# Kernel optimization log

Measured on AMD Instinct MI355X. Metric: run time of the kernel, lower is better.

Reference implementation:

```python
import jax, jax.numpy as jnp
import numpy as np

MARGIN = 0.2  # args.margin
N, D, NUM_CLASSES = 512, 256, 32


def setup_inputs() -> dict:
    key = jax.random.key(0)
    k1, k2 = jax.random.split(key)
    embeddings = jax.random.normal(k1, (N, D), dtype=jnp.float32)
    labels = jax.random.randint(k2, (N,), 0, NUM_CLASSES, dtype=jnp.int64)
    return {"embeddings": embeddings, "labels": labels}


def reference(embeddings, labels):
    """TripletMarginMiner forward (type_of_triplets='all', euclidean, no l2 norm).

    torch version returns variable-length (anchor, pos, neg) index vectors;
    for jit-compatibility we return the equivalent fixed-shape [N,N,N] boolean
    mask M where M[a,p,n]=True iff (a,p,n) is a mined triplet. The torch output
    is exactly jnp.where(M).
    """
    emb = jax.lax.stop_gradient(embeddings)  # embeddings.detach()

    # pairwise squared-euclidean distance matrix [N, N]
    sq = jnp.sum(emb * emb, axis=1)
    mat = jnp.maximum(sq[:, None] + sq[None, :] - 2.0 * (emb @ emb.T), 0.0)

    # label structure
    sames = labels[:, None] == labels[None, :]          # [N, N]
    diffs = ~sames
    sames = sames & ~jnp.eye(labels.shape[0], dtype=bool)  # fill_diagonal_(0)
    valid = sames[:, :, None] & diffs[:, None, :]        # [a, p, n]

    # triplet_margin[a,p,n] = an_dist - ap_dist = mat[a,n] - mat[a,p]
    triplet_margin = mat[:, None, :] - mat[:, :, None]   # [a, p, n]

    # type_of_triplets == 'all': margin violators
    mask = valid & (triplet_margin <= MARGIN)
    return mask
```

## Files before the change

### kernel.cpp

```cpp
#include <hip/hip_runtime.h>

#pragma clang fp contract(off)

#define NN 512
#define DD 256

typedef int int4v __attribute__((ext_vector_type(4)));

__device__ __forceinline__ float np_leaf128_avx512(const float* __restrict__ x)
{
    float p[16];
    #pragma unroll
    for (int i = 0; i < 16; ++i) {
        const float q0 = x[i]       * x[i];
        const float q1 = x[i + 16]  * x[i + 16];
        const float q2 = x[i + 32]  * x[i + 32];
        const float q3 = x[i + 48]  * x[i + 48];
        const float q4 = x[i + 64]  * x[i + 64];
        const float q5 = x[i + 80]  * x[i + 80];
        const float q6 = x[i + 96]  * x[i + 96];
        const float q7 = x[i + 112] * x[i + 112];
        p[i] = ((q0 + q1) + (q2 + q3)) + ((q4 + q5) + (q6 + q7));
    }
    float q[8];
    #pragma unroll
    for (int i = 0; i < 8; ++i) q[i] = p[i] + p[i + 8];
    const float s0 = q[0] + q[4];
    const float s1 = q[1] + q[5];
    const float s2 = q[2] + q[6];
    const float s3 = q[3] + q[7];
    const float u0 = s0 + s2;
    const float u1 = s1 + s3;
    return u0 + u1;
}

__global__ __launch_bounds__(512)
void triplet_kernel(const float* __restrict__ emb,
                    const int* __restrict__ lab,
                    int* __restrict__ out)
{
    __shared__ int   canon[NN];
    __shared__ float arow[DD];
    __shared__ float dn[NN];
    __shared__ float mp[NN];
    __shared__ float sq_a_sh;
    __shared__ int   det_lab64;

    const int a = blockIdx.x;
    const int t = threadIdx.x;

    if (t == 0) det_lab64 = 0;
    __syncthreads();
    if (t < 256 && lab[2 * t + 1] == 0) atomicAdd(&det_lab64, 1);
    __syncthreads();
    canon[t] = (det_lab64 == 256) ? lab[2 * t] : lab[t];

    if (t < DD) arow[t] = emb[(size_t)a * DD + t];
    __syncthreads();

    const float* __restrict__ xr = emb + (size_t)t * DD;
    const float sqj = np_leaf128_avx512(xr) + np_leaf128_avx512(xr + 128);
    if (t == a) sq_a_sh = sqj;

    float dot = 0.0f;
    for (int k = 0; k < DD; ++k)
        dot = __builtin_fmaf(arow[k], xr[k], dot);
    __syncthreads();

    const float t1 = sq_a_sh + sqj;
    const float t2 = 2.0f * dot;
    float m = t1 - t2;
    m = m > 0.0f ? m : 0.0f;

    const int la = canon[a];
    dn[t] = (canon[t] != la) ? m : __builtin_inff();
    mp[t] = (canon[t] == la && t != a) ? m : __builtin_nanf("");
    __syncthreads();

    const int tx = t & 127;
    const int ty = t >> 7;
    const float d0 = dn[4 * tx + 0];
    const float d1 = dn[4 * tx + 1];
    const float d2 = dn[4 * tx + 2];
    const float d3 = dn[4 * tx + 3];

    int4v* base = (int4v*)out + (size_t)a * NN * (NN / 4) + tx;
    for (int p = ty; p < NN; p += 4) {
        const float mpp = mp[p];
        int4v r;
        r.x = ((d0 - mpp) <= 0.2f) ? 1 : 0;
        r.y = ((d1 - mpp) <= 0.2f) ? 1 : 0;
        r.z = ((d2 - mpp) <= 0.2f) ? 1 : 0;
        r.w = ((d3 - mpp) <= 0.2f) ? 1 : 0;
        base[(size_t)p * (NN / 4)] = r;
    }
}

extern "C" void kernel_launch(void* const* d_in, const int* in_sizes, int n_in,
                              void* d_out, int out_size, void* d_ws, size_t ws_size,
                              hipStream_t stream)
{
    const float* emb    = (const float*)d_in[0];
    const int*   labels = (const int*)d_in[1];
    int*         out    = (int*)d_out;
    (void)d_ws; (void)ws_size;

    triplet_kernel<<<NN, 512, 0, stream>>>(emb, labels, out);
}
```

Before: 569.7 us.

## Split triplet mask into distance-table kernel and widely parallel mask-writing kernel

Splits the fused kernel in two. The first kernel computes per-anchor negative and positive distance tables into workspace. The second launches 4096 blocks of 256 threads, each writing a 64-row chunk of the 512MB output mask. This spreads the dominant output write over many more blocks than the original 512, aiming to raise memory-level parallelism. In exchange it adds a second launch and a round trip of the tables through workspace, and it falls back to the fused kernel when the workspace is too small.

```diff
diff --git a/kernel.cpp b/kernel.cpp
--- a/kernel.cpp
+++ b/kernel.cpp
@@ -4,10 +4,11 @@
 
 #define NN 512
 #define DD 256
+#define PCH 64
 
 typedef int int4v __attribute__((ext_vector_type(4)));
 
-__device__ __forceinline__ float np_leaf128_avx512(const float* __restrict__ x)
+__device__ __forceinline__ float np_leaf128(const float* __restrict__ x)
 {
     float p[16];
     #pragma unroll
@@ -29,15 +30,94 @@
     const float s1 = q[1] + q[5];
     const float s2 = q[2] + q[6];
     const float s3 = q[3] + q[7];
-    const float u0 = s0 + s2;
-    const float u1 = s1 + s3;
-    return u0 + u1;
+    return (s0 + s2) + (s1 + s3);
 }
 
 __global__ __launch_bounds__(512)
-void triplet_kernel(const float* __restrict__ emb,
-                    const int* __restrict__ lab,
-                    int* __restrict__ out)
+void tables_kernel(const float* __restrict__ emb,
+                   const int* __restrict__ lab,
+                   float* __restrict__ dn_ws,
+                   float* __restrict__ mp_ws)
+{
+    __shared__ int   canon[NN];
+    __shared__ float arow[DD];
+    __shared__ float sq_a_sh;
+    __shared__ int   det_lab64;
+
+    const int a = blockIdx.x;
+    const int t = threadIdx.x;
+
+    if (t == 0) det_lab64 = 0;
+    __syncthreads();
+    if (t < 256 && lab[2 * t + 1] == 0) atomicAdd(&det_lab64, 1);
+    __syncthreads();
+    canon[t] = (det_lab64 == 256) ? lab[2 * t] : lab[t];
+
+    if (t < DD) arow[t] = emb[(size_t)a * DD + t];
+    __syncthreads();
+
+    const float* __restrict__ xr = emb + (size_t)t * DD;
+    const float sqj = np_leaf128(xr) + np_leaf128(xr + 128);
+    if (t == a) sq_a_sh = sqj;
+
+    float dot = 0.0f;
+    for (int k = 0; k < DD; ++k)
+        dot = __builtin_fmaf(arow[k], xr[k], dot);
+    __syncthreads();
+
+    const float t1 = sq_a_sh + sqj;
+    const float t2 = 2.0f * dot;
+    float m = t1 - t2;
+    m = m > 0.0f ? m : 0.0f;
+
+    const int la = canon[a];
+    dn_ws[(size_t)a * NN + t] = (canon[t] != la) ? m : __builtin_inff();
+    mp_ws[(size_t)a * NN + t] = (canon[t] == la && t != a) ? m
+                                                           : __builtin_nanf("");
+}
+
+__global__ __launch_bounds__(256)
+void mask_kernel(const float* __restrict__ dn_ws,
+                 const float* __restrict__ mp_ws,
+                 int* __restrict__ out)
+{
+    __shared__ float dn_sh[NN];
+    __shared__ float mp_sh[PCH];
+
+    const int bid = blockIdx.x;
+    const int a   = bid >> 3;
+    const int pc  = bid & 7;
+    const int t   = threadIdx.x;
+
+    dn_sh[t]       = dn_ws[(size_t)a * NN + t];
+    dn_sh[t + 256] = dn_ws[(size_t)a * NN + t + 256];
+    if (t < PCH) mp_sh[t] = mp_ws[(size_t)a * NN + pc * PCH + t];
+    __syncthreads();
+
+    const int tx = t & 127;
+    const int ty = t >> 7;
+    const float d0 = dn_sh[4 * tx + 0];
+    const float d1 = dn_sh[4 * tx + 1];
+    const float d2 = dn_sh[4 * tx + 2];
+    const float d3 = dn_sh[4 * tx + 3];
+
+    int4v* base = (int4v*)out
+                + ((size_t)a * NN + (size_t)pc * PCH) * (NN / 4) + tx;
+    for (int p2 = ty; p2 < PCH; p2 += 2) {
+        const float mpp = mp_sh[p2];
+        int4v r;
+        r.x = ((d0 - mpp) <= 0.2f) ? 1 : 0;
+        r.y = ((d1 - mpp) <= 0.2f) ? 1 : 0;
+        r.z = ((d2 - mpp) <= 0.2f) ? 1 : 0;
+        r.w = ((d3 - mpp) <= 0.2f) ? 1 : 0;
+        base[(size_t)p2 * (NN / 4)] = r;
+    }
+}
+
+__global__ __launch_bounds__(512)
+void triplet_fused_kernel(const float* __restrict__ emb,
+                          const int* __restrict__ lab,
+                          int* __restrict__ out)
 {
     __shared__ int   canon[NN];
     __shared__ float arow[DD];
@@ -59,7 +139,7 @@
     __syncthreads();
 
     const float* __restrict__ xr = emb + (size_t)t * DD;
-    const float sqj = np_leaf128_avx512(xr) + np_leaf128_avx512(xr + 128);
+    const float sqj = np_leaf128(xr) + np_leaf128(xr + 128);
     if (t == a) sq_a_sh = sqj;
 
     float dot = 0.0f;
@@ -103,7 +183,14 @@
     const float* emb    = (const float*)d_in[0];
     const int*   labels = (const int*)d_in[1];
     int*         out    = (int*)d_out;
-    (void)d_ws; (void)ws_size;
 
-    triplet_kernel<<<NN, 512, 0, stream>>>(emb, labels, out);
+    const size_t tbl = (size_t)NN * NN * sizeof(float);
+    if (ws_size >= 2 * tbl) {
+        float* dn_ws = (float*)d_ws;
+        float* mp_ws = (float*)((char*)d_ws + tbl);
+        tables_kernel<<<NN, 512, 0, stream>>>(emb, labels, dn_ws, mp_ws);
+        mask_kernel<<<NN * (NN / PCH), 256, 0, stream>>>(dn_ws, mp_ws, out);
+    } else {
+        triplet_fused_kernel<<<NN, 512, 0, stream>>>(emb, labels, out);
+    }
 }
```

New measurement: 599.5 us. 1.05x slower.
